# Performance work log

Measured on AMD Instinct MI355X. Metric: run time of the kernel, lower is better.

## Reference

```python
import jax, jax.numpy as jnp
import numpy as np

H, FFN, E, TOPK = 1024, 4096, 8, 2
B, S = 2, 1024


def setup_inputs() -> dict:
    key = jax.random.key(0)
    k1, k2, k3, k4 = jax.random.split(key, 4)
    s_h = 1.0 / np.sqrt(H).astype(np.float32)
    s_f = 1.0 / np.sqrt(FFN).astype(np.float32)
    return {
        "hidden_states": jax.random.normal(k1, (B, S, H), jnp.float32),
        "gate_w": jax.random.normal(k2, (E, H), jnp.float32) * s_h,       # router Linear(H->E), no bias
        "w13": jax.random.normal(k3, (E, 2 * FFN, H), jnp.float32) * s_h,  # fused [w1; w3] per expert
        "w2": jax.random.normal(k4, (E, H, FFN), jnp.float32) * s_f,       # down-proj per expert
        "top_k": TOPK,
    }


def reference(hidden_states, gate_w, w13, w2, top_k):
    b, s, h = hidden_states.shape
    x = hidden_states.reshape(-1, h)                       # [T, H]
    router_logits = x @ gate_w.T                           # [T, E]
    rw = jax.nn.softmax(router_logits.astype(jnp.float32), axis=1)
    rw, sel = jax.lax.top_k(rw, top_k)                     # [T, K] each
    rw = rw / rw.sum(axis=-1, keepdims=True)
    rw = rw.astype(x.dtype)
    e_tot = gate_w.shape[0]
    f = w2.shape[2]
    # combine[t, e] = sum_k rw[t, k] * (sel[t, k] == e)
    combine = jnp.sum((sel[..., None] == jnp.arange(e_tot)) * rw[..., None], axis=1)  # [T, E]
    out = jnp.zeros_like(x)
    for e in range(e_tot):  # static small loop over experts
        g = x @ w13[e, :f].T            # [T, F] gate proj
        u = x @ w13[e, f:].T            # [T, F] up proj
        y = (jax.nn.silu(g) * u) @ w2[e].T  # [T, H]
        out = out + combine[:, e:e + 1] * y
    return out.reshape(b, s, h), router_logits
```

## Files before the change

kernel.cpp:

```cpp
#include <hip/hip_runtime.h>
#include <hip/hip_bf16.h>
#include <math.h>

#define H     1024
#define FFN   4096
#define NE    8
#define TOK   2048
#define PAIRS (TOK*2)
#define BM    128
#define BK    32
#define ROWCAP (PAIRS + NE*BM)
#define MAXTILES (ROWCAP/BM)
#define AT    (BM*BK)

typedef unsigned short u16;
typedef __attribute__((ext_vector_type(8))) __bf16 bf16x8;
typedef __attribute__((ext_vector_type(4))) float  f32x4;

__device__ __forceinline__ unsigned cvt2(float a, float b) {
    __hip_bfloat162 h = __float22bfloat162_rn(float2{a, b});
    unsigned u;
    __builtin_memcpy(&u, &h, 4);
    return u;
}

#define GLD16(gp, lp) __builtin_amdgcn_global_load_lds( \
    (const __attribute__((address_space(1))) void*)(gp), \
    (__attribute__((address_space(3))) void*)(lp), 16, 0, 0)

#define PIPE_BARRIER() do { \
    asm volatile("s_waitcnt vmcnt(6) lgkmcnt(0)" ::: "memory"); \
    __builtin_amdgcn_s_barrier(); \
} while (0)

__global__ void k_init(int* counts) {
    if (threadIdx.x < NE) counts[threadIdx.x] = 0;
}

__global__ void k_router(const float* __restrict__ x, const float* __restrict__ gw,
                         float* __restrict__ logits, int* counts,
                         int* __restrict__ sel, int* __restrict__ posn, float* __restrict__ wgt) {
    int lane = threadIdx.x & 63;
    int t = blockIdx.x * 4 + (threadIdx.x >> 6);
    float p[NE];
#pragma unroll
    for (int e = 0; e < NE; e++) p[e] = 0.f;
    for (int j = 0; j < H / 64; j++) {
        int h = lane + j * 64;
        float xv = x[(size_t)t * H + h];
#pragma unroll
        for (int e = 0; e < NE; e++) p[e] = fmaf(xv, gw[e * H + h], p[e]);
    }
#pragma unroll
    for (int off = 32; off; off >>= 1)
#pragma unroll
        for (int e = 0; e < NE; e++) p[e] += __shfl_xor(p[e], off, 64);
    if (lane == 0) {
        float mx = p[0];
#pragma unroll
        for (int e = 1; e < NE; e++) mx = fmaxf(mx, p[e]);
        float pe[NE];
#pragma unroll
        for (int e = 0; e < NE; e++) pe[e] = __expf(p[e] - mx);
        int i0 = 0;
#pragma unroll
        for (int e = 1; e < NE; e++) if (pe[e] > pe[i0]) i0 = e;
        int i1 = (i0 == 0) ? 1 : 0;
#pragma unroll
        for (int e = 0; e < NE; e++) if (e != i1 && e != i0 && pe[e] > pe[i1]) i1 = e;
        float w0 = pe[i0] / (pe[i0] + pe[i1]);
#pragma unroll
        for (int e = 0; e < NE; e++) logits[(size_t)t * NE + e] = p[e];
        int p0 = atomicAdd(&counts[i0], 1);
        int p1 = atomicAdd(&counts[i1], 1);
        sel[2 * t] = i0;  posn[2 * t] = p0;  wgt[2 * t] = w0;
        sel[2 * t + 1] = i1;  posn[2 * t + 1] = p1;  wgt[2 * t + 1] = 1.f - w0;
    }
}

__global__ void k_prefix(const int* __restrict__ counts, int* __restrict__ base,
                         int* __restrict__ tile_e) {
    if (threadIdx.x == 0) {
        int b = 0, tb = 0;
        for (int e = 0; e < NE; e++) {
            base[e] = b;
            int nt = (counts[e] + BM - 1) / BM;
            for (int i = 0; i < nt; i++) tile_e[tb++] = e;
            b += nt * BM;
        }
        base[NE] = b;
        while (tb < MAXTILES) tile_e[tb++] = -1;
    }
}

__global__ void k_gather(const float4* __restrict__ x4, const int* __restrict__ sel,
                         const int* __restrict__ posn, const int* __restrict__ base,
                         u16* __restrict__ xg) {
    int p = blockIdx.x;
    int lane = threadIdx.x;
    int t = p >> 1;
    int row = base[sel[p]] + posn[p];
    int f2 = ((row >> 1) & 3) << 1;
#pragma unroll
    for (int i = 0; i < 4; i++) {
        int idx = i * 64 + lane;
        float4 v = x4[(size_t)t * (H / 4) + (idx ^ f2)];
        uint2 o = { cvt2(v.x, v.y), cvt2(v.z, v.w) };
        *(uint2*)&xg[(size_t)row * H + idx * 4] = o;
    }
}

__global__ __launch_bounds__(256) void k_gemm1(const u16* __restrict__ xg,
                                               const float* __restrict__ w13,
                                               u16* __restrict__ act,
                                               const int* __restrict__ tile_e) {
    int id = blockIdx.x;
    int xcd = id & 7;
    int j = id >> 3;
    int tile = j % MAXTILES;
    int n0i = xcd * 8 + j / MAXTILES;
    int e = tile_e[tile];
    if (e < 0) return;
    __shared__ u16 As[3][AT];
    __shared__ u16 Bs[2][2][64 * (BK + 8)];

    int tid = threadIdx.x;
    int lane = tid & 63, wave = tid >> 6;
    int quad = lane >> 4, m16 = lane & 15;
    int wm = wave >> 1, wn = wave & 1;
    int row0 = tile * BM;
    int n0 = n0i * 64;
    const float* wb1 = w13 + ((size_t)e * 2 * FFN + n0) * H;
    const float* wb3 = w13 + ((size_t)e * 2 * FFN + FFN + n0) * H;

    f32x4 accg[4][2], accu[4][2];
#pragma unroll
    for (int mi = 0; mi < 4; mi++)
#pragma unroll
        for (int ni = 0; ni < 2; ni++) { accg[mi][ni] = {0.f,0.f,0.f,0.f}; accu[mi][ni] = {0.f,0.f,0.f,0.f}; }

    const int NT = H / BK;
    float4 v1a[2], v3a[2], v1b[2], v3b[2];
    int ia0 = 0, ia1 = 1, ia2 = 2;
    int aslot = quad ^ ((m16 >> 1) & 3);

#pragma unroll
    for (int i = 0; i < 2; i++) {
        int chunk = i * 256 + tid;
        GLD16(xg + (size_t)(row0 + (chunk >> 2)) * H + (chunk & 3) * 8, As[0] + chunk * 8);
    }
#pragma unroll
    for (int i = 0; i < 2; i++) {
        int idx = i * 256 + tid;
        v1a[i] = *(const float4*)(wb1 + (size_t)(idx >> 3) * H + (idx & 7) * 4);
        v3a[i] = *(const float4*)(wb3 + (size_t)(idx >> 3) * H + (idx & 7) * 4);
    }
#pragma unroll
    for (int i = 0; i < 2; i++) {
        int chunk = i * 256 + tid;
        GLD16(xg + (size_t)(row0 + (chunk >> 2)) * H + BK + (chunk & 3) * 8, As[1] + chunk * 8);
    }
#pragma unroll
    for (int i = 0; i < 2; i++) {
        int idx = i * 256 + tid;
        v1b[i] = *(const float4*)(wb1 + (size_t)(idx >> 3) * H + BK + (idx & 7) * 4);
        v3b[i] = *(const float4*)(wb3 + (size_t)(idx >> 3) * H + BK + (idx & 7) * 4);
    }
#pragma unroll
    for (int i = 0; i < 2; i++) {
        int idx = i * 256 + tid;
        int r = idx >> 3, c4 = idx & 7;
        uint2 o1 = { cvt2(v1a[i].x, v1a[i].y), cvt2(v1a[i].z, v1a[i].w) };
        uint2 o3 = { cvt2(v3a[i].x, v3a[i].y), cvt2(v3a[i].z, v3a[i].w) };
        *(uint2*)&Bs[0][0][r * (BK + 8) + c4 * 4] = o1;
        *(uint2*)&Bs[0][1][r * (BK + 8) + c4 * 4] = o3;
    }
    PIPE_BARRIER();

#define G1_STEP(IT, V1L, V3L, V1C, V3C, BC, BN)                                             \
    {                                                                                       \
        int itp2 = (IT) + 2;                                                                \
        if (itp2 < NT) {                                                                    \
            int kk = itp2 * BK;                                                             \
            _Pragma("unroll")                                                               \
            for (int i = 0; i < 2; i++) {                                                   \
                int chunk = i * 256 + tid;                                                  \
                GLD16(xg + (size_t)(row0 + (chunk >> 2)) * H + kk + (chunk & 3) * 8,        \
                      As[ia2] + chunk * 8);                                                 \
            }                                                                               \
            _Pragma("unroll")                                                               \
            for (int i = 0; i < 2; i++) {                                                   \
                int idx = i * 256 + tid;                                                    \
                V1L[i] = *(const float4*)(wb1 + (size_t)(idx >> 3) * H + kk + (idx & 7) * 4);\
                V3L[i] = *(const float4*)(wb3 + (size_t)(idx >> 3) * H + kk + (idx & 7) * 4);\
            }                                                                               \
        }                                                                                   \
        bf16x8 a[4], bg[2], bu[2];                                                          \
        _Pragma("unroll")                                                                   \
        for (int mi = 0; mi < 4; mi++)                                                      \
            a[mi] = *(const bf16x8*)&As[ia0][(wm * 64 + mi * 16 + m16) * BK + aslot * 8];   \
        _Pragma("unroll")                                                                   \
        for (int ni = 0; ni < 2; ni++) {                                                    \
            bg[ni] = *(const bf16x8*)&Bs[BC][0][(wn * 32 + ni * 16 + m16) * (BK + 8) + quad * 8];\
            bu[ni] = *(const bf16x8*)&Bs[BC][1][(wn * 32 + ni * 16 + m16) * (BK + 8) + quad * 8];\
        }                                                                                   \
        _Pragma("unroll")                                                                   \
        for (int mi = 0; mi < 4; mi++)                                                      \
            _Pragma("unroll")                                                               \
            for (int ni = 0; ni < 2; ni++) {                                                \
                accg[mi][ni] = __builtin_amdgcn_mfma_f32_16x16x32_bf16(a[mi], bg[ni], accg[mi][ni], 0, 0, 0);\
                accu[mi][ni] = __builtin_amdgcn_mfma_f32_16x16x32_bf16(a[mi], bu[ni], accu[mi][ni], 0, 0, 0);\
            }                                                                               \
        __builtin_amdgcn_sched_barrier(0);                                                  \
        if ((IT) + 1 < NT) {                                                                \
            _Pragma("unroll")                                                               \
            for (int i = 0; i < 2; i++) {                                                   \
                int idx = i * 256 + tid;                                                    \
                int r = idx >> 3, c4 = idx & 7;                                             \
                uint2 o1 = { cvt2(V1C[i].x, V1C[i].y), cvt2(V1C[i].z, V1C[i].w) };          \
                uint2 o3 = { cvt2(V3C[i].x, V3C[i].y), cvt2(V3C[i].z, V3C[i].w) };          \
                *(uint2*)&Bs[BN][0][r * (BK + 8) + c4 * 4] = o1;                            \
                *(uint2*)&Bs[BN][1][r * (BK + 8) + c4 * 4] = o3;                            \
            }                                                                               \
        }                                                                                   \
        PIPE_BARRIER();                                                                     \
        int rot = ia0; ia0 = ia1; ia1 = ia2; ia2 = rot;                                     \
    }

    for (int it = 0; it < NT; it += 2) {
        G1_STEP(it,     v1a, v3a, v1b, v3b, 0, 1);
        G1_STEP(it + 1, v1b, v3b, v1a, v3a, 1, 0);
    }
#undef G1_STEP

#pragma unroll
    for (int mi = 0; mi < 4; mi++)
#pragma unroll
        for (int ni = 0; ni < 2; ni++) {
            int gcol = n0 + wn * 32 + ni * 16 + m16;
            int grow = row0 + wm * 64 + mi * 16 + quad * 4;
#pragma unroll
            for (int r = 0; r < 4; r++) {
                float g = accg[mi][ni][r], u = accu[mi][ni][r];
                float hv = g * (1.f / (1.f + __expf(-g))) * u;
                int f = ((quad * 4 + r) >> 1) & 3;
                act[(size_t)(grow + r) * FFN + (gcol ^ (f << 3))] = (u16)(cvt2(hv, hv) & 0xffff);
            }
        }
}

__global__ __launch_bounds__(256) void k_gemm2(const u16* __restrict__ act,
                                               const float* __restrict__ w2,
                                               float* __restrict__ yc,
                                               const int* __restrict__ tile_e) {
    int id = blockIdx.x;
    int xcd = id & 7;
    int j = id >> 3;
    int tile = j % MAXTILES;
    int pz = xcd * 2 + j / MAXTILES;
    int e = tile_e[tile];
    if (e < 0) return;
    __shared__ u16 As[3][AT];
    __shared__ u16 Bs[2][BM * (BK + 8)];

    int tid = threadIdx.x;
    int lane = tid & 63, wave = tid >> 6;
    int quad = lane >> 4, m16 = lane & 15;
    int wm = wave >> 1, wn = wave & 1;
    int row0 = tile * BM;
    int n0 = (pz >> 1) * 128;
    int z = pz & 1;
    int k0 = z * (FFN / 2);
    const float* wb = w2 + ((size_t)e * H + n0) * FFN;
    float* ycp = yc + (size_t)z * ROWCAP * H;

    f32x4 acc[4][4];
#pragma unroll
    for (int mi = 0; mi < 4; mi++)
#pragma unroll
        for (int ni = 0; ni < 4; ni++) acc[mi][ni] = {0.f,0.f,0.f,0.f};

    const int NT = (FFN / 2) / BK;
    float4 va[4], vb[4];
    int ia0 = 0, ia1 = 1, ia2 = 2;
    int aslot = quad ^ ((m16 >> 1) & 3);

#pragma unroll
    for (int i = 0; i < 2; i++) {
        int chunk = i * 256 + tid;
        GLD16(act + (size_t)(row0 + (chunk >> 2)) * FFN + k0 + (chunk & 3) * 8, As[0] + chunk * 8);
    }
#pragma unroll
    for (int i = 0; i < 4; i++) {
        int idx = i * 256 + tid;
        va[i] = *(const float4*)(wb + (size_t)(idx >> 3) * FFN + k0 + (idx & 7) * 4);
    }
#pragma unroll
    for (int i = 0; i < 2; i++) {
        int chunk = i * 256 + tid;
        GLD16(act + (size_t)(row0 + (chunk >> 2)) * FFN + k0 + BK + (chunk & 3) * 8, As[1] + chunk * 8);
    }
#pragma unroll
    for (int i = 0; i < 4; i++) {
        int idx = i * 256 + tid;
        vb[i] = *(const float4*)(wb + (size_t)(idx >> 3) * FFN + k0 + BK + (idx & 7) * 4);
    }
#pragma unroll
    for (int i = 0; i < 4; i++) {
        int idx = i * 256 + tid;
        int r = idx >> 3, c4 = idx & 7;
        uint2 o = { cvt2(va[i].x, va[i].y), cvt2(va[i].z, va[i].w) };
        *(uint2*)&Bs[0][r * (BK + 8) + c4 * 4] = o;
    }
    PIPE_BARRIER();

#define G2_STEP(IT, VL, VC, BC, BN)                                                         \
    {                                                                                       \
        int itp2 = (IT) + 2;                                                                \
        if (itp2 < NT) {                                                                    \
            int kk = k0 + itp2 * BK;                                                        \
            _Pragma("unroll")                                                               \
            for (int i = 0; i < 2; i++) {                                                   \
                int chunk = i * 256 + tid;                                                  \
                GLD16(act + (size_t)(row0 + (chunk >> 2)) * FFN + kk + (chunk & 3) * 8,     \
                      As[ia2] + chunk * 8);                                                 \
            }                                                                               \
            _Pragma("unroll")                                                               \
            for (int i = 0; i < 4; i++) {                                                   \
                int idx = i * 256 + tid;                                                    \
                VL[i] = *(const float4*)(wb + (size_t)(idx >> 3) * FFN + kk + (idx & 7) * 4);\
            }                                                                               \
        }                                                                                   \
        bf16x8 a[4], b[4];                                                                  \
        _Pragma("unroll")                                                                   \
        for (int mi = 0; mi < 4; mi++)                                                      \
            a[mi] = *(const bf16x8*)&As[ia0][(wm * 64 + mi * 16 + m16) * BK + aslot * 8];   \
        _Pragma("unroll")                                                                   \
        for (int ni = 0; ni < 4; ni++)                                                      \
            b[ni] = *(const bf16x8*)&Bs[BC][(wn * 64 + ni * 16 + m16) * (BK + 8) + quad * 8];\
        _Pragma("unroll")                                                                   \
        for (int mi = 0; mi < 4; mi++)                                                      \
            _Pragma("unroll")                                                               \
            for (int ni = 0; ni < 4; ni++)                                                  \
                acc[mi][ni] = __builtin_amdgcn_mfma_f32_16x16x32_bf16(a[mi], b[ni], acc[mi][ni], 0, 0, 0);\
        __builtin_amdgcn_sched_barrier(0);                                                  \
        if ((IT) + 1 < NT) {                                                                \
            _Pragma("unroll")                                                               \
            for (int i = 0; i < 4; i++) {                                                   \
                int idx = i * 256 + tid;                                                    \
                int r = idx >> 3, c4 = idx & 7;                                             \
                uint2 o = { cvt2(VC[i].x, VC[i].y), cvt2(VC[i].z, VC[i].w) };               \
                *(uint2*)&Bs[BN][r * (BK + 8) + c4 * 4] = o;                                \
            }                                                                               \
        }                                                                                   \
        PIPE_BARRIER();                                                                     \
        int rot = ia0; ia0 = ia1; ia1 = ia2; ia2 = rot;                                     \
    }

    for (int it = 0; it < NT; it += 2) {
        G2_STEP(it,     va, vb, 0, 1);
        G2_STEP(it + 1, vb, va, 1, 0);
    }
#undef G2_STEP

#pragma unroll
    for (int mi = 0; mi < 4; mi++)
#pragma unroll
        for (int ni = 0; ni < 4; ni++)
#pragma unroll
            for (int r = 0; r < 4; r++) {
                int grow = row0 + wm * 64 + mi * 16 + quad * 4 + r;
                int gcol = n0 + wn * 64 + ni * 16 + m16;
                ycp[(size_t)grow * H + gcol] = acc[mi][ni][r];
            }
}

__global__ void k_combine(const float4* __restrict__ yc4, const int* __restrict__ sel,
                          const int* __restrict__ posn, const int* __restrict__ base,
                          const float* __restrict__ wgt, float4* __restrict__ out4) {
    int t = blockIdx.x;
    int j = threadIdx.x;
    int r0 = base[sel[2 * t]] + posn[2 * t];
    int r1 = base[sel[2 * t + 1]] + posn[2 * t + 1];
    float w0 = wgt[2 * t], w1 = wgt[2 * t + 1];
    const size_t P = (size_t)ROWCAP * (H / 4);
    float4 a0 = yc4[(size_t)r0 * (H / 4) + j];
    float4 a1 = yc4[(size_t)r0 * (H / 4) + j + P];
    float4 b0 = yc4[(size_t)r1 * (H / 4) + j];
    float4 b1 = yc4[(size_t)r1 * (H / 4) + j + P];
    float4 o = { w0 * (a0.x + a1.x) + w1 * (b0.x + b1.x),
                 w0 * (a0.y + a1.y) + w1 * (b0.y + b1.y),
                 w0 * (a0.z + a1.z) + w1 * (b0.z + b1.z),
                 w0 * (a0.w + a1.w) + w1 * (b0.w + b1.w) };
    out4[(size_t)t * (H / 4) + j] = o;
}

extern "C" void kernel_launch(void* const* d_in, const int* in_sizes, int n_in,
                              void* d_out, int out_size, void* d_ws, size_t ws_size,
                              hipStream_t stream) {
    const float* x   = (const float*)d_in[0];
    const float* gw  = (const float*)d_in[1];
    const float* w13 = (const float*)d_in[2];
    const float* w2  = (const float*)d_in[3];
    float* out    = (float*)d_out;
    float* logits = out + (size_t)TOK * H;

    char* ws = (char*)d_ws;
    int*   counts = (int*)ws;
    int*   base   = (int*)(ws + 256);
    int*   tile_e = (int*)(ws + 512);
    int*   sel    = (int*)(ws + 1024);
    int*   posn   = (int*)(ws + 1024 + 4 * PAIRS);
    float* wgt    = (float*)(ws + 1024 + 8 * PAIRS);
    u16*   xg     = (u16*)(ws + 65536);
    u16*   act    = xg + (size_t)ROWCAP * H;
    float* yc     = (float*)(act + (size_t)ROWCAP * FFN);

    k_init<<<1, 64, 0, stream>>>(counts);
    k_router<<<TOK / 4, 256, 0, stream>>>(x, gw, logits, counts, sel, posn, wgt);
    k_prefix<<<1, 64, 0, stream>>>(counts, base, tile_e);
    k_gather<<<PAIRS, 64, 0, stream>>>((const float4*)x, sel, posn, base, xg);
    k_gemm1<<<dim3(MAXTILES * (FFN / 64)), 256, 0, stream>>>(xg, w13, act, tile_e);
    k_gemm2<<<dim3(MAXTILES * (H / 128) * 2), 256, 0, stream>>>(act, w2, yc, tile_e);
    k_combine<<<TOK, 256, 0, stream>>>((const float4*)yc, sel, posn, base, wgt, (float4*)out);
}
```

Measured before the change: 786.6 us.

## Reduce A-tile LDS buffering to double buffer with explicit vmcnt waits

Both grouped GEMM kernels move from a triple-buffered A tile with a uniform barrier to double-buffered A and B tiles, using named static LDS buffers. A is now prefetched only one step ahead via global_load_lds, and hand-tuned s_waitcnt vmcnt values control when the converted B tile is written and when the barrier runs. The last two iterations are peeled off to drop the prefetch branches. This cuts LDS footprint (possibly raising occupancy) and removes dynamic buffer-index rotation, but leaves less time to hide A load latency and depends on exact counts of outstanding loads being correct.

```diff
diff --git a/kernel.cpp b/kernel.cpp
--- a/kernel.cpp
+++ b/kernel.cpp
@@ -28,10 +28,6 @@
     (const __attribute__((address_space(1))) void*)(gp), \
     (__attribute__((address_space(3))) void*)(lp), 16, 0, 0)
 
-#define PIPE_BARRIER() do { \
-    asm volatile("s_waitcnt vmcnt(6) lgkmcnt(0)" ::: "memory"); \
-    __builtin_amdgcn_s_barrier(); \
-} while (0)
 
 __global__ void k_init(int* counts) {
     if (threadIdx.x < NE) counts[threadIdx.x] = 0;
@@ -121,8 +117,9 @@
     int n0i = xcd * 8 + j / MAXTILES;
     int e = tile_e[tile];
     if (e < 0) return;
-    __shared__ u16 As[3][AT];
-    __shared__ u16 Bs[2][2][64 * (BK + 8)];
+    __shared__ u16 As0[AT], As1[AT];
+    __shared__ u16 B1s0[64 * (BK + 8)], B3s0[64 * (BK + 8)];
+    __shared__ u16 B1s1[64 * (BK + 8)], B3s1[64 * (BK + 8)];
 
     int tid = threadIdx.x;
     int lane = tid & 63, wave = tid >> 6;
@@ -141,24 +138,19 @@
 
     const int NT = H / BK;
     float4 v1a[2], v3a[2], v1b[2], v3b[2];
-    int ia0 = 0, ia1 = 1, ia2 = 2;
     int aslot = quad ^ ((m16 >> 1) & 3);
 
 #pragma unroll
     for (int i = 0; i < 2; i++) {
         int chunk = i * 256 + tid;
-        GLD16(xg + (size_t)(row0 + (chunk >> 2)) * H + (chunk & 3) * 8, As[0] + chunk * 8);
-    }
+        GLD16(xg + (size_t)(row0 + (chunk >> 2)) * H + (chunk & 3) * 8, As0 + chunk * 8);
+    }
+    asm volatile("" ::: "memory");
 #pragma unroll
     for (int i = 0; i < 2; i++) {
         int idx = i * 256 + tid;
         v1a[i] = *(const float4*)(wb1 + (size_t)(idx >> 3) * H + (idx & 7) * 4);
         v3a[i] = *(const float4*)(wb3 + (size_t)(idx >> 3) * H + (idx & 7) * 4);
-    }
-#pragma unroll
-    for (int i = 0; i < 2; i++) {
-        int chunk = i * 256 + tid;
-        GLD16(xg + (size_t)(row0 + (chunk >> 2)) * H + BK + (chunk & 3) * 8, As[1] + chunk * 8);
     }
 #pragma unroll
     for (int i = 0; i < 2; i++) {
@@ -172,65 +164,77 @@
         int r = idx >> 3, c4 = idx & 7;
         uint2 o1 = { cvt2(v1a[i].x, v1a[i].y), cvt2(v1a[i].z, v1a[i].w) };
         uint2 o3 = { cvt2(v3a[i].x, v3a[i].y), cvt2(v3a[i].z, v3a[i].w) };
-        *(uint2*)&Bs[0][0][r * (BK + 8) + c4 * 4] = o1;
-        *(uint2*)&Bs[0][1][r * (BK + 8) + c4 * 4] = o3;
-    }
-    PIPE_BARRIER();
-
-#define G1_STEP(IT, V1L, V3L, V1C, V3C, BC, BN)                                             \
+        *(uint2*)&B1s0[r * (BK + 8) + c4 * 4] = o1;
+        *(uint2*)&B3s0[r * (BK + 8) + c4 * 4] = o3;
+    }
+    asm volatile("s_waitcnt vmcnt(4)" ::: "memory");
+    asm volatile("s_waitcnt lgkmcnt(0)" ::: "memory");
+    __builtin_amdgcn_s_barrier();
+
+#define G1_STEP(IT, ASC, ASN, BGC, BUC, BGN, BUN, V1L, V3L, V1C, V3C, PFB, PFA, WA, WB)     \
     {                                                                                       \
-        int itp2 = (IT) + 2;                                                                \
-        if (itp2 < NT) {                                                                    \
-            int kk = itp2 * BK;                                                             \
+        if (PFA) {                                                                          \
+            int ka = ((IT) + 1) * BK;                                                       \
             _Pragma("unroll")                                                               \
             for (int i = 0; i < 2; i++) {                                                   \
                 int chunk = i * 256 + tid;                                                  \
-                GLD16(xg + (size_t)(row0 + (chunk >> 2)) * H + kk + (chunk & 3) * 8,        \
-                      As[ia2] + chunk * 8);                                                 \
-            }                                                                               \
+                GLD16(xg + (size_t)(row0 + (chunk >> 2)) * H + ka + (chunk & 3) * 8,        \
+                      ASN + chunk * 8);                                                     \
+            }                                                                               \
+        }                                                                                   \
+        asm volatile("" ::: "memory");                                                      \
+        if (PFB) {                                                                          \
+            int kb = ((IT) + 2) * BK;                                                       \
             _Pragma("unroll")                                                               \
             for (int i = 0; i < 2; i++) {                                                   \
                 int idx = i * 256 + tid;                                                    \
-                V1L[i] = *(const float4*)(wb1 + (size_t)(idx >> 3) * H + kk + (idx & 7) * 4);\
-                V3L[i] = *(const float4*)(wb3 + (size_t)(idx >> 3) * H + kk + (idx & 7) * 4);\
-            }                                                                               \
-        }                                                                                   \
-        bf16x8 a[4], bg[2], bu[2];                                                          \
-        _Pragma("unroll")                                                                   \
-        for (int mi = 0; mi < 4; mi++)                                                      \
-            a[mi] = *(const bf16x8*)&As[ia0][(wm * 64 + mi * 16 + m16) * BK + aslot * 8];   \
-        _Pragma("unroll")                                                                   \
-        for (int ni = 0; ni < 2; ni++) {                                                    \
-            bg[ni] = *(const bf16x8*)&Bs[BC][0][(wn * 32 + ni * 16 + m16) * (BK + 8) + quad * 8];\
-            bu[ni] = *(const bf16x8*)&Bs[BC][1][(wn * 32 + ni * 16 + m16) * (BK + 8) + quad * 8];\
-        }                                                                                   \
-        _Pragma("unroll")                                                                   \
-        for (int mi = 0; mi < 4; mi++)                                                      \
+                V1L[i] = *(const float4*)(wb1 + (size_t)(idx >> 3) * H + kb + (idx & 7) * 4);\
+                V3L[i] = *(const float4*)(wb3 + (size_t)(idx >> 3) * H + kb + (idx & 7) * 4);\
+            }                                                                               \
+        }                                                                                   \
+        __builtin_amdgcn_sched_barrier(0);                                                  \
+        {                                                                                   \
+            bf16x8 a[4], bg[2], bu[2];                                                      \
+            _Pragma("unroll")                                                               \
+            for (int mi = 0; mi < 4; mi++)                                                  \
+                a[mi] = *(const bf16x8*)&ASC[(wm * 64 + mi * 16 + m16) * BK + aslot * 8];   \
             _Pragma("unroll")                                                               \
             for (int ni = 0; ni < 2; ni++) {                                                \
-                accg[mi][ni] = __builtin_amdgcn_mfma_f32_16x16x32_bf16(a[mi], bg[ni], accg[mi][ni], 0, 0, 0);\
-                accu[mi][ni] = __builtin_amdgcn_mfma_f32_16x16x32_bf16(a[mi], bu[ni], accu[mi][ni], 0, 0, 0);\
-            }                                                                               \
-        __builtin_amdgcn_sched_barrier(0);                                                  \
-        if ((IT) + 1 < NT) {                                                                \
+                bg[ni] = *(const bf16x8*)&BGC[(wn * 32 + ni * 16 + m16) * (BK + 8) + quad * 8];\
+                bu[ni] = *(const bf16x8*)&BUC[(wn * 32 + ni * 16 + m16) * (BK + 8) + quad * 8];\
+            }                                                                               \
+            _Pragma("unroll")                                                               \
+            for (int mi = 0; mi < 4; mi++)                                                  \
+                _Pragma("unroll")                                                           \
+                for (int ni = 0; ni < 2; ni++) {                                            \
+                    accg[mi][ni] = __builtin_amdgcn_mfma_f32_16x16x32_bf16(a[mi], bg[ni], accg[mi][ni], 0, 0, 0);\
+                    accu[mi][ni] = __builtin_amdgcn_mfma_f32_16x16x32_bf16(a[mi], bu[ni], accu[mi][ni], 0, 0, 0);\
+                }                                                                           \
+        }                                                                                   \
+        if (PFA) {                                                                          \
+            asm volatile("s_waitcnt vmcnt(" WA ")" ::: "memory");                           \
+            __builtin_amdgcn_sched_barrier(0);                                              \
             _Pragma("unroll")                                                               \
             for (int i = 0; i < 2; i++) {                                                   \
                 int idx = i * 256 + tid;                                                    \
                 int r = idx >> 3, c4 = idx & 7;                                             \
                 uint2 o1 = { cvt2(V1C[i].x, V1C[i].y), cvt2(V1C[i].z, V1C[i].w) };          \
                 uint2 o3 = { cvt2(V3C[i].x, V3C[i].y), cvt2(V3C[i].z, V3C[i].w) };          \
-                *(uint2*)&Bs[BN][0][r * (BK + 8) + c4 * 4] = o1;                            \
-                *(uint2*)&Bs[BN][1][r * (BK + 8) + c4 * 4] = o3;                            \
-            }                                                                               \
-        }                                                                                   \
-        PIPE_BARRIER();                                                                     \
-        int rot = ia0; ia0 = ia1; ia1 = ia2; ia2 = rot;                                     \
-    }
-
-    for (int it = 0; it < NT; it += 2) {
-        G1_STEP(it,     v1a, v3a, v1b, v3b, 0, 1);
-        G1_STEP(it + 1, v1b, v3b, v1a, v3a, 1, 0);
-    }
+                *(uint2*)&BGN[r * (BK + 8) + c4 * 4] = o1;                                  \
+                *(uint2*)&BUN[r * (BK + 8) + c4 * 4] = o3;                                  \
+            }                                                                               \
+            asm volatile("s_waitcnt vmcnt(" WB ")" ::: "memory");                           \
+        }                                                                                   \
+        asm volatile("s_waitcnt lgkmcnt(0)" ::: "memory");                                  \
+        __builtin_amdgcn_s_barrier();                                                       \
+    }
+
+    for (int it = 0; it < NT - 2; it += 2) {
+        G1_STEP(it,     As0, As1, B1s0, B3s0, B1s1, B3s1, v1a, v3a, v1b, v3b, true, true, "6", "4");
+        G1_STEP(it + 1, As1, As0, B1s1, B3s1, B1s0, B3s0, v1b, v3b, v1a, v3a, true, true, "6", "4");
+    }
+    G1_STEP(NT - 2, As0, As1, B1s0, B3s0, B1s1, B3s1, v1a, v3a, v1b, v3b, false, true,  "2", "0");
+    G1_STEP(NT - 1, As1, As0, B1s1, B3s1, B1s0, B3s0, v1b, v3b, v1a, v3a, false, false, "0", "0");
 #undef G1_STEP
 
 #pragma unroll
@@ -260,8 +264,8 @@
     int pz = xcd * 2 + j / MAXTILES;
     int e = tile_e[tile];
     if (e < 0) return;
-    __shared__ u16 As[3][AT];
-    __shared__ u16 Bs[2][BM * (BK + 8)];
+    __shared__ u16 As0[AT], As1[AT];
+    __shared__ u16 Bs0[BM * (BK + 8)], Bs1[BM * (BK + 8)];
 
     int tid = threadIdx.x;
     int lane = tid & 63, wave = tid >> 6;
@@ -282,23 +286,18 @@
 
     const int NT = (FFN / 2) / BK;
     float4 va[4], vb[4];
-    int ia0 = 0, ia1 = 1, ia2 = 2;
     int aslot = quad ^ ((m16 >> 1) & 3);
 
 #pragma unroll
     for (int i = 0; i < 2; i++) {
         int chunk = i * 256 + tid;
-        GLD16(act + (size_t)(row0 + (chunk >> 2)) * FFN + k0 + (chunk & 3) * 8, As[0] + chunk * 8);
-    }
+        GLD16(act + (size_t)(row0 + (chunk >> 2)) * FFN + k0 + (chunk & 3) * 8, As0 + chunk * 8);
+    }
+    asm volatile("" ::: "memory");
 #pragma unroll
     for (int i = 0; i < 4; i++) {
         int idx = i * 256 + tid;
         va[i] = *(const float4*)(wb + (size_t)(idx >> 3) * FFN + k0 + (idx & 7) * 4);
-    }
-#pragma unroll
-    for (int i = 0; i < 2; i++) {
-        int chunk = i * 256 + tid;
-        GLD16(act + (size_t)(row0 + (chunk >> 2)) * FFN + k0 + BK + (chunk & 3) * 8, As[1] + chunk * 8);
     }
 #pragma unroll
     for (int i = 0; i < 4; i++) {
@@ -310,57 +309,69 @@
         int idx = i * 256 + tid;
         int r = idx >> 3, c4 = idx & 7;
         uint2 o = { cvt2(va[i].x, va[i].y), cvt2(va[i].z, va[i].w) };
-        *(uint2*)&Bs[0][r * (BK + 8) + c4 * 4] = o;
-    }
-    PIPE_BARRIER();
-
-#define G2_STEP(IT, VL, VC, BC, BN)                                                         \
+        *(uint2*)&Bs0[r * (BK + 8) + c4 * 4] = o;
+    }
+    asm volatile("s_waitcnt vmcnt(4)" ::: "memory");
+    asm volatile("s_waitcnt lgkmcnt(0)" ::: "memory");
+    __builtin_amdgcn_s_barrier();
+
+#define G2_STEP(IT, ASC, ASN, BSC, BSN, VL, VC, PFB, PFA, WA, WB)                           \
     {                                                                                       \
-        int itp2 = (IT) + 2;                                                                \
-        if (itp2 < NT) {                                                                    \
-            int kk = k0 + itp2 * BK;                                                        \
+        if (PFA) {                                                                          \
+            int ka = k0 + ((IT) + 1) * BK;                                                  \
             _Pragma("unroll")                                                               \
             for (int i = 0; i < 2; i++) {                                                   \
                 int chunk = i * 256 + tid;                                                  \
-                GLD16(act + (size_t)(row0 + (chunk >> 2)) * FFN + kk + (chunk & 3) * 8,     \
-                      As[ia2] + chunk * 8);                                                 \
-            }                                                                               \
+                GLD16(act + (size_t)(row0 + (chunk >> 2)) * FFN + ka + (chunk & 3) * 8,     \
+                      ASN + chunk * 8);                                                     \
+            }                                                                               \
+        }                                                                                   \
+        asm volatile("" ::: "memory");                                                      \
+        if (PFB) {                                                                          \
+            int kb = k0 + ((IT) + 2) * BK;                                                  \
             _Pragma("unroll")                                                               \
             for (int i = 0; i < 4; i++) {                                                   \
                 int idx = i * 256 + tid;                                                    \
-                VL[i] = *(const float4*)(wb + (size_t)(idx >> 3) * FFN + kk + (idx & 7) * 4);\
-            }                                                                               \
-        }                                                                                   \
-        bf16x8 a[4], b[4];                                                                  \
-        _Pragma("unroll")                                                                   \
-        for (int mi = 0; mi < 4; mi++)                                                      \
-            a[mi] = *(const bf16x8*)&As[ia0][(wm * 64 + mi * 16 + m16) * BK + aslot * 8];   \
-        _Pragma("unroll")                                                                   \
-        for (int ni = 0; ni < 4; ni++)                                                      \
-            b[ni] = *(const bf16x8*)&Bs[BC][(wn * 64 + ni * 16 + m16) * (BK + 8) + quad * 8];\
-        _Pragma("unroll")                                                                   \
-        for (int mi = 0; mi < 4; mi++)                                                      \
+                VL[i] = *(const float4*)(wb + (size_t)(idx >> 3) * FFN + kb + (idx & 7) * 4);\
+            }                                                                               \
+        }                                                                                   \
+        __builtin_amdgcn_sched_barrier(0);                                                  \
+        {                                                                                   \
+            bf16x8 a[4], b[4];                                                              \
+            _Pragma("unroll")                                                               \
+            for (int mi = 0; mi < 4; mi++)                                                  \
+                a[mi] = *(const bf16x8*)&ASC[(wm * 64 + mi * 16 + m16) * BK + aslot * 8];   \
             _Pragma("unroll")                                                               \
             for (int ni = 0; ni < 4; ni++)                                                  \
-                acc[mi][ni] = __builtin_amdgcn_mfma_f32_16x16x32_bf16(a[mi], b[ni], acc[mi][ni], 0, 0, 0);\
-        __builtin_amdgcn_sched_barrier(0);                                                  \
-        if ((IT) + 1 < NT) {                                                                \
+                b[ni] = *(const bf16x8*)&BSC[(wn * 64 + ni * 16 + m16) * (BK + 8) + quad * 8];\
+            _Pragma("unroll")                                                               \
+            for (int mi = 0; mi < 4; mi++)                                                  \
+                _Pragma("unroll")                                                           \
+                for (int ni = 0; ni < 4; ni++)                                              \
+                    acc[mi][ni] = __builtin_amdgcn_mfma_f32_16x16x32_bf16(a[mi], b[ni], acc[mi][ni], 0, 0, 0);\
+        }                                                                                   \
+        if (PFA) {                                                                          \
+            asm volatile("s_waitcnt vmcnt(" WA ")" ::: "memory");                           \
+            __builtin_amdgcn_sched_barrier(0);                                              \
             _Pragma("unroll")                                                               \
             for (int i = 0; i < 4; i++) {                                                   \
                 int idx = i * 256 + tid;                                                    \
                 int r = idx >> 3, c4 = idx & 7;                                             \
                 uint2 o = { cvt2(VC[i].x, VC[i].y), cvt2(VC[i].z, VC[i].w) };               \
-                *(uint2*)&Bs[BN][r * (BK + 8) + c4 * 4] = o;                                \
-            }                                                                               \
-        }                                                                                   \
-        PIPE_BARRIER();                                                                     \
-        int rot = ia0; ia0 = ia1; ia1 = ia2; ia2 = rot;                                     \
-    }
-
-    for (int it = 0; it < NT; it += 2) {
-        G2_STEP(it,     va, vb, 0, 1);
-        G2_STEP(it + 1, vb, va, 1, 0);
-    }
+                *(uint2*)&BSN[r * (BK + 8) + c4 * 4] = o;                                   \
+            }                                                                               \
+            asm volatile("s_waitcnt vmcnt(" WB ")" ::: "memory");                           \
+        }                                                                                   \
+        asm volatile("s_waitcnt lgkmcnt(0)" ::: "memory");                                  \
+        __builtin_amdgcn_s_barrier();                                                       \
+    }
+
+    for (int it = 0; it < NT - 2; it += 2) {
+        G2_STEP(it,     As0, As1, Bs0, Bs1, va, vb, true, true, "6", "4");
+        G2_STEP(it + 1, As1, As0, Bs1, Bs0, vb, va, true, true, "6", "4");
+    }
+    G2_STEP(NT - 2, As0, As1, Bs0, Bs1, va, vb, false, true,  "2", "0");
+    G2_STEP(NT - 1, As1, As0, Bs1, Bs0, vb, va, false, false, "0", "0");
 #undef G2_STEP
 
 #pragma unroll
```

New measurement: 719.6 us. 1.09x faster.
